# Kernel tuning notes

Hardware: AMD Instinct MI355X
Metric: run time of the kernel (lower is better)

Reference implementation:

```python
import jax, jax.numpy as jnp
import numpy as np

N_NODES = 100000
D = 256
E = 1000000
H = 128


def setup_inputs() -> dict:
    key = jax.random.key(0)
    k1, k2, k3, k4 = jax.random.split(key, 4)
    z = jax.random.normal(k1, (N_NODES, D), dtype=jnp.float32)
    edge_label_index = jax.random.randint(k2, (2, E), 0, N_NODES, dtype=jnp.int64)
    # Linear layers: PyTorch Linear(in, out) -> weight [out, in]; stored here as [in, out].
    W1 = jax.random.normal(k3, (2 * D, H), dtype=jnp.float32) * (1.0 / np.sqrt(2 * D))
    b1 = jnp.zeros((H,), dtype=jnp.float32)
    W2 = jax.random.normal(k4, (H, 1), dtype=jnp.float32) * (1.0 / np.sqrt(H))
    b2 = jnp.zeros((1,), dtype=jnp.float32)
    return {"z": z, "edge_label_index": edge_label_index,
            "W1": W1, "b1": b1, "W2": W2, "b2": b2}


def reference(z, edge_label_index, W1, b1, W2, b2):
    src = edge_label_index[0]
    dst = edge_label_index[1]
    # Gather node pairs and concat: [E, 2*D]
    pair = jnp.concatenate([z[src], z[dst]], axis=-1)
    h = jax.nn.relu(pair @ W1 + b1)          # [E, H]
    out = (h @ W2 + b2).reshape(-1)          # [E]
    return out
```

## Files before the change

### kernel.cpp

```cpp
#include <hip/hip_runtime.h>
#include <hip/hip_bf16.h>


typedef __attribute__((ext_vector_type(4))) float floatx4;
typedef __attribute__((ext_vector_type(8))) short short8;
typedef _Float16 half8v __attribute__((ext_vector_type(8)));

__device__ __forceinline__ unsigned short bf16rne(float x) {
    unsigned int u = __float_as_uint(x);
    u += 0x7fffu + ((u >> 16) & 1u);
    return (unsigned short)(u >> 16);
}

__device__ __forceinline__ void gl_lds16(const void* g, void* l) {
    __builtin_amdgcn_global_load_lds(
        (const __attribute__((address_space(1))) void*)(unsigned long long)g,
        (__attribute__((address_space(3))) void*)(unsigned)(unsigned long long)l,
        16, 0, 0);
}

__global__ void cvt_w1h(const float* __restrict__ W1, unsigned short* __restrict__ BTc2) {
    int t = blockIdx.x * blockDim.x + threadIdx.x;
    int hf = t >> 15, rem = t & 32767;
    int s = rem >> 12, rem2 = rem & 4095;
    int n = rem2 >> 5, rem3 = rem2 & 31;
    int gp = rem3 >> 3, j = rem3 & 7;
    int g = gp ^ ((n >> 1) & 3);
    int k = hf * 256 + s * 32 + g * 8 + j;
    BTc2[t] = bf16rne(W1[k * 128 + n]);
}

__global__ void cvt_w1(const float* __restrict__ W1, unsigned short* __restrict__ BTc) {
    int t = blockIdx.x * blockDim.x + threadIdx.x;
    int s = t >> 12, rem = t & 4095;
    int n = rem >> 5, rem2 = rem & 31;
    int gp = rem2 >> 3, j = rem2 & 7;
    int g = gp ^ ((n >> 1) & 3);
    int k = s * 32 + g * 8 + j;
    BTc[t] = bf16rne(W1[k * 128 + n]);
}

__global__ __launch_bounds__(256, 2)
void gemm_hb(const float* __restrict__ zf, int nnodes,
             const unsigned short* __restrict__ BTc2,
             const float* __restrict__ b1, _Float16* __restrict__ Hh)
{
    __shared__ unsigned short btile[2][2][2][128][32];

    const int t = threadIdx.x;
    const int wid = t >> 6;
    const int lane = t & 63;
    const int l15 = lane & 15;
    const int quad = lane >> 4;
    const int m0 = blockIdx.x * 128 + wid * 32;

    unsigned offs[2];
#pragma unroll
    for (int mf = 0; mf < 2; ++mf) {
        int r = m0 + mf * 16 + l15;
        r = r < nnodes ? r : nnodes - 1;
        offs[mf] = (unsigned)r * 1024u;
    }
    const char* zbb = (const char*)zf;

    const int swz = (l15 >> 1) & 3;
    const unsigned short* bbase = &btile[0][0][0][0][0] + l15 * 32 + (quad ^ swz) * 8;

    auto stage = [&](int kc, int buf) {
        char* lbase = (char*)&btile[0][0][0][0][0] + buf * 32768 + wid * 1024 + lane * 16;
        const char* gbase = (const char*)BTc2 + kc * 16384 + wid * 1024 + lane * 16;
#pragma unroll
        for (int h = 0; h < 2; ++h) {
            const char* g = gbase + h * 65536;
            char* l = lbase + h * 16384;
#pragma unroll
            for (int i = 0; i < 4; ++i)
                gl_lds16(g + i * 4096, l + i * 4096);
        }
    };

    auto load_a = [&](int ks, short8* dst) {
        const int cb = ks * 128 + quad * 32;
#pragma unroll
        for (int mf = 0; mf < 2; ++mf) {
            const float* pf = (const float*)(zbb + (size_t)offs[mf] + cb);
            float4 f0 = *(const float4*)pf;
            float4 f1 = *(const float4*)(pf + 4);
            short8 av;
            av[0] = (short)bf16rne(f0.x); av[1] = (short)bf16rne(f0.y);
            av[2] = (short)bf16rne(f0.z); av[3] = (short)bf16rne(f0.w);
            av[4] = (short)bf16rne(f1.x); av[5] = (short)bf16rne(f1.y);
            av[6] = (short)bf16rne(f1.z); av[7] = (short)bf16rne(f1.w);
            dst[mf] = av;
        }
    };

    floatx4 acc[2][16];
#pragma unroll
    for (int mf = 0; mf < 2; ++mf)
#pragma unroll
        for (int nf = 0; nf < 16; ++nf)
            acc[mf][nf] = (floatx4){0.f, 0.f, 0.f, 0.f};

    short8 A[3][2];
    stage(0, 0);
    load_a(0, A[0]);
    load_a(1, A[1]);
    __syncthreads();

#pragma unroll
    for (int kc = 0; kc < 4; ++kc) {
        if (kc < 3) stage(kc + 1, (kc + 1) & 1);

#pragma unroll
        for (int s4 = 0; s4 < 2; ++s4) {
            const int ks = kc * 2 + s4;
            if (ks + 2 < 8) load_a(ks + 2, A[(ks + 2) % 3]);

            const unsigned short* bs0 = bbase + (kc & 1) * 16384 + s4 * 4096;
            const short8* ac = A[ks % 3];

#pragma unroll
            for (int gq = 0; gq < 4; ++gq) {
                const unsigned short* bs = bs0 + (gq >> 1) * 8192 + (gq & 1) * 2048;
                short8 bfr[4];
#pragma unroll
                for (int nf = 0; nf < 4; ++nf)
                    bfr[nf] = *(const short8*)(bs + nf * 512);
#pragma unroll
                for (int nf = 0; nf < 4; ++nf)
#pragma unroll
                    for (int mf = 0; mf < 2; ++mf)
                        acc[mf][gq * 4 + nf] = __builtin_amdgcn_mfma_f32_16x16x32_bf16(
                            ac[mf], bfr[nf], acc[mf][gq * 4 + nf], 0, 0, 0);
            }
        }

        if (kc < 3) __syncthreads();
    }

    float b1v[8];
#pragma unroll
    for (int nf = 0; nf < 8; ++nf)
        b1v[nf] = b1[nf * 16 + l15];
#pragma unroll
    for (int mf = 0; mf < 2; ++mf) {
#pragma unroll
        for (int r = 0; r < 4; ++r) {
            int row = m0 + mf * 16 + quad * 4 + r;
            if (row < nnodes) {
                _Float16* hp = Hh + (size_t)row * 256 + l15;
#pragma unroll
                for (int nf = 0; nf < 8; ++nf)
                    hp[nf * 16] = (_Float16)(acc[mf][nf][r] + b1v[nf]);
#pragma unroll
                for (int nf = 0; nf < 8; ++nf)
                    hp[128 + nf * 16] = (_Float16)acc[mf][8 + nf][r];
            }
        }
    }
}

__global__ __launch_bounds__(256)
void edge_out(const _Float16* __restrict__ Hh, const int* __restrict__ eli,
              int E, int nnodes,
              const float* __restrict__ W2, const float* __restrict__ b2,
              float* __restrict__ out)
{
    const int t = threadIdx.x;
    const int lane = t & 63;
    const int wid = t >> 6;
    const int l15 = lane & 15;
    const int grp = lane >> 4;

    float w2v[8];
#pragma unroll
    for (int j = 0; j < 8; ++j)
        w2v[j] = W2[l15 * 8 + j];
    const float b2s = b2[0];

    const int e0 = blockIdx.x * 64 + wid * 16 + grp;

    half8v hs[4], hd[4];
    int ee[4];
#pragma unroll
    for (int i = 0; i < 4; ++i) {
        int e = e0 + i * 4;
        ee[i] = e;
        int ec = e < E ? e : E - 1;
        int s = eli[ec];
        int d = eli[E + ec];
        s = s < 0 ? 0 : (s >= nnodes ? nnodes - 1 : s);
        d = d < 0 ? 0 : (d >= nnodes ? nnodes - 1 : d);
        hs[i] = *(const half8v*)(Hh + (size_t)s * 256 + l15 * 8);
        hd[i] = *(const half8v*)(Hh + (size_t)d * 256 + 128 + l15 * 8);
    }
#pragma unroll
    for (int i = 0; i < 4; ++i) {
        float sacc = 0.f;
#pragma unroll
        for (int j = 0; j < 8; ++j) {
            float v = (float)hs[i][j] + (float)hd[i][j];
            v = v > 0.f ? v : 0.f;
            sacc = fmaf(v, w2v[j], sacc);
        }
        sacc += __shfl_xor(sacc, 1);
        sacc += __shfl_xor(sacc, 2);
        sacc += __shfl_xor(sacc, 4);
        sacc += __shfl_xor(sacc, 8);
        if (l15 == 0 && ee[i] < E)
            out[ee[i]] = sacc + b2s;
    }
}

__global__ __launch_bounds__(256, 2)
void fused_mlp_f32(const float* __restrict__ zf, const int* __restrict__ eli,
                   int E, int nnodes,
                   const unsigned short* __restrict__ BTc,
                   const float* __restrict__ b1, const float* __restrict__ W2,
                   const float* __restrict__ b2, float* __restrict__ out)
{
    __shared__ unsigned short btile[2][4][128][32];

    const int t = threadIdx.x;
    const int wid = t >> 6;
    const int lane = t & 63;
    const int l15 = lane & 15;
    const int quad = lane >> 4;
    const int m0 = blockIdx.x * 256 + wid * 64;

    unsigned offs[4], offd[4];
#pragma unroll
    for (int mf = 0; mf < 4; ++mf) {
        int e = m0 + mf * 16 + l15;
        e = e < E ? e : E - 1;
        int s = eli[e];
        int d = eli[E + e];
        s = s < 0 ? 0 : (s >= nnodes ? nnodes - 1 : s);
        d = d < 0 ? 0 : (d >= nnodes ? nnodes - 1 : d);
        offs[mf] = (unsigned)s * 1024u;
        offd[mf] = (unsigned)d * 1024u;
    }
    const char* zbb = (const char*)zf;

    const int swz = (l15 >> 1) & 3;
    const unsigned short* bbase = &btile[0][0][0][0] + l15 * 32 + (quad ^ swz) * 8;

    auto stage = [&](int kc, int buf) {
        const char* g = (const char*)BTc + kc * 32768 + wid * 1024 + lane * 16;
        char* l = (char*)&btile[buf][0][0][0] + wid * 1024 + lane * 16;
#pragma unroll
        for (int i = 0; i < 8; ++i)
            gl_lds16(g + i * 4096, l + i * 4096);
    };

    auto load_a = [&](int ks, short8* dst) {
        const unsigned* off = (ks < 8) ? offs : offd;
        const int cb = (ks & 7) * 128 + quad * 32;
#pragma unroll
        for (int mf = 0; mf < 4; ++mf) {
            const float* pf = (const float*)(zbb + (size_t)off[mf] + cb);
            float4 f0 = *(const float4*)pf;
            float4 f1 = *(const float4*)(pf + 4);
            short8 av;
            av[0] = (short)bf16rne(f0.x); av[1] = (short)bf16rne(f0.y);
            av[2] = (short)bf16rne(f0.z); av[3] = (short)bf16rne(f0.w);
            av[4] = (short)bf16rne(f1.x); av[5] = (short)bf16rne(f1.y);
            av[6] = (short)bf16rne(f1.z); av[7] = (short)bf16rne(f1.w);
            dst[mf] = av;
        }
    };

    floatx4 acc[4][8];
#pragma unroll
    for (int mf = 0; mf < 4; ++mf)
#pragma unroll
        for (int nf = 0; nf < 8; ++nf)
            acc[mf][nf] = (floatx4){0.f, 0.f, 0.f, 0.f};

    short8 A[3][4];
    stage(0, 0);
    load_a(0, A[0]);
    load_a(1, A[1]);
    __syncthreads();

#pragma unroll
    for (int kc = 0; kc < 4; ++kc) {
        if (kc < 3) stage(kc + 1, (kc + 1) & 1);

#pragma unroll
        for (int s4 = 0; s4 < 4; ++s4) {
            const int ks = kc * 4 + s4;
            if (ks + 2 < 16) load_a(ks + 2, A[(ks + 2) % 3]);

            const unsigned short* bs = bbase + (kc & 1) * 16384 + s4 * 4096;
            short8 bfr[8];
#pragma unroll
            for (int nf = 0; nf < 8; ++nf)
                bfr[nf] = *(const short8*)(bs + nf * 512);

            const short8* ac = A[ks % 3];
#pragma unroll
            for (int nf = 0; nf < 8; ++nf)
#pragma unroll
                for (int mf = 0; mf < 4; ++mf)
                    acc[mf][nf] = __builtin_amdgcn_mfma_f32_16x16x32_bf16(
                        ac[mf], bfr[nf], acc[mf][nf], 0, 0, 0);
        }

        if (kc < 3) __syncthreads();
    }

    const float b2s = b2[0];
    float b1v[8], w2v[8];
#pragma unroll
    for (int nf = 0; nf < 8; ++nf) {
        int c = nf * 16 + l15;
        b1v[nf] = b1[c];
        w2v[nf] = W2[c];
    }
#pragma unroll
    for (int mf = 0; mf < 4; ++mf) {
#pragma unroll
        for (int r = 0; r < 4; ++r) {
            float s = 0.f;
#pragma unroll
            for (int nf = 0; nf < 8; ++nf) {
                float v = acc[mf][nf][r] + b1v[nf];
                v = v > 0.f ? v : 0.f;
                s = fmaf(v, w2v[nf], s);
            }
            s += __shfl_xor(s, 1);
            s += __shfl_xor(s, 2);
            s += __shfl_xor(s, 4);
            s += __shfl_xor(s, 8);
            if (l15 == 0) {
                int e = m0 + mf * 16 + quad * 4 + r;
                if (e < E) out[e] = s + b2s;
            }
        }
    }
}

__global__ void naive_edge(const float* __restrict__ z, const int* __restrict__ eli,
                           int E, int nnodes,
                           const float* __restrict__ W1, const float* __restrict__ b1,
                           const float* __restrict__ W2, const float* __restrict__ b2,
                           float* __restrict__ out)
{
    __shared__ float red[2];
    int e = blockIdx.x;
    int j = threadIdx.x;
    int s = eli[e], d = eli[E + e];
    s = s < 0 ? 0 : (s >= nnodes ? nnodes - 1 : s);
    d = d < 0 ? 0 : (d >= nnodes ? nnodes - 1 : d);
    const float* zs = z + (long long)s * 256;
    const float* zd = z + (long long)d * 256;
    float h = b1[j];
    for (int i = 0; i < 256; ++i) h = fmaf(zs[i], W1[i * 128 + j], h);
    for (int i = 0; i < 256; ++i) h = fmaf(zd[i], W1[(256 + i) * 128 + j], h);
    h = h > 0.f ? h : 0.f;
    float v = h * W2[j];
    v += __shfl_xor(v, 1);  v += __shfl_xor(v, 2);  v += __shfl_xor(v, 4);
    v += __shfl_xor(v, 8);  v += __shfl_xor(v, 16); v += __shfl_xor(v, 32);
    if ((threadIdx.x & 63) == 0) red[threadIdx.x >> 6] = v;
    __syncthreads();
    if (threadIdx.x == 0) out[e] = red[0] + red[1] + b2[0];
}

extern "C" void kernel_launch(void* const* d_in, const int* in_sizes, int n_in,
                              void* d_out, int out_size, void* d_ws, size_t ws_size,
                              hipStream_t stream) {
    const float* z   = (const float*)d_in[0];
    const int*   eli = (const int*)d_in[1];
    const float* W1  = (const float*)d_in[2];
    const float* b1  = (const float*)d_in[3];
    const float* W2  = (const float*)d_in[4];
    const float* b2  = (const float*)d_in[5];
    float*       out = (float*)d_out;

    const int E      = in_sizes[1] / 2;
    const int nnodes = in_sizes[0] / 256;

    const size_t HB   = (size_t)nnodes * 512;
    const size_t BT2B = 131072;
    const size_t BTB  = (size_t)512 * 128 * 2;

    const int grid_gemm = (nnodes + 127) / 128;
    const int grid_edge = (E + 63) / 64;

    if (ws_size >= HB + BT2B) {
        _Float16*       Hh   = (_Float16*)d_ws;
        unsigned short* BTc2 = (unsigned short*)((char*)d_ws + HB);
        cvt_w1h<<<256, 256, 0, stream>>>(W1, BTc2);
        gemm_hb<<<grid_gemm, 256, 0, stream>>>(z, nnodes, BTc2, b1, Hh);
        edge_out<<<grid_edge, 256, 0, stream>>>(Hh, eli, E, nnodes, W2, b2, out);
    } else if (ws_size >= BTB) {
        unsigned short* BTc = (unsigned short*)d_ws;
        cvt_w1<<<256, 256, 0, stream>>>(W1, BTc);
        fused_mlp_f32<<<(E + 255) / 256, 256, 0, stream>>>(z, eli, E, nnodes, BTc, b1, W2, b2, out);
    } else {
        naive_edge<<<E, 128, 0, stream>>>(z, eli, E, nnodes, W1, b1, W2, b2, out);
    }
}
```

Baseline: 247.1 us.

## Read W1 fragments directly from global and use packed fp16 dot in edge kernel

The node GEMM stops staging the bf16 W1 tiles into LDS with async global-to-LDS copies and barriers. Each wave now loads its B fragments straight from global memory, relying on the small weight being L2/L1 resident, and deepens the A prefetch ring to four stages. The edge kernel does the add and relu in packed fp16 and accumulates with fdot2 against fp16-converted W2. This removes LDS traffic and syncs but adds redundant global loads per wave. It also lowers precision, since the add, relu and W2 now run in fp16.

```diff
diff --git a/kernel.cpp b/kernel.cpp
--- a/kernel.cpp
+++ b/kernel.cpp
@@ -5,6 +5,13 @@
 typedef __attribute__((ext_vector_type(4))) float floatx4;
 typedef __attribute__((ext_vector_type(8))) short short8;
 typedef _Float16 half8v __attribute__((ext_vector_type(8)));
+typedef __fp16 fp16x2 __attribute__((ext_vector_type(2)));
+
+#if defined(__has_builtin)
+#if __has_builtin(__builtin_amdgcn_fdot2)
+#define HAVE_FDOT2 1
+#endif
+#endif
 
 __device__ __forceinline__ unsigned short bf16rne(float x) {
     unsigned int u = __float_as_uint(x);
@@ -45,8 +52,6 @@
              const unsigned short* __restrict__ BTc2,
              const float* __restrict__ b1, _Float16* __restrict__ Hh)
 {
-    __shared__ unsigned short btile[2][2][2][128][32];
-
     const int t = threadIdx.x;
     const int wid = t >> 6;
     const int lane = t & 63;
@@ -64,20 +69,7 @@
     const char* zbb = (const char*)zf;
 
     const int swz = (l15 >> 1) & 3;
-    const unsigned short* bbase = &btile[0][0][0][0][0] + l15 * 32 + (quad ^ swz) * 8;
-
-    auto stage = [&](int kc, int buf) {
-        char* lbase = (char*)&btile[0][0][0][0][0] + buf * 32768 + wid * 1024 + lane * 16;
-        const char* gbase = (const char*)BTc2 + kc * 16384 + wid * 1024 + lane * 16;
-#pragma unroll
-        for (int h = 0; h < 2; ++h) {
-            const char* g = gbase + h * 65536;
-            char* l = lbase + h * 16384;
-#pragma unroll
-            for (int i = 0; i < 4; ++i)
-                gl_lds16(g + i * 4096, l + i * 4096);
-        }
-    };
+    const unsigned short* gb = BTc2 + l15 * 32 + (quad ^ swz) * 8;
 
     auto load_a = [&](int ks, short8* dst) {
         const int cb = ks * 128 + quad * 32;
@@ -102,41 +94,32 @@
         for (int nf = 0; nf < 16; ++nf)
             acc[mf][nf] = (floatx4){0.f, 0.f, 0.f, 0.f};
 
-    short8 A[3][2];
-    stage(0, 0);
+    short8 A[4][2];
     load_a(0, A[0]);
     load_a(1, A[1]);
-    __syncthreads();
-
-#pragma unroll
-    for (int kc = 0; kc < 4; ++kc) {
-        if (kc < 3) stage(kc + 1, (kc + 1) & 1);
-
-#pragma unroll
-        for (int s4 = 0; s4 < 2; ++s4) {
-            const int ks = kc * 2 + s4;
-            if (ks + 2 < 8) load_a(ks + 2, A[(ks + 2) % 3]);
-
-            const unsigned short* bs0 = bbase + (kc & 1) * 16384 + s4 * 4096;
-            const short8* ac = A[ks % 3];
-
-#pragma unroll
-            for (int gq = 0; gq < 4; ++gq) {
-                const unsigned short* bs = bs0 + (gq >> 1) * 8192 + (gq & 1) * 2048;
-                short8 bfr[4];
-#pragma unroll
-                for (int nf = 0; nf < 4; ++nf)
-                    bfr[nf] = *(const short8*)(bs + nf * 512);
-#pragma unroll
-                for (int nf = 0; nf < 4; ++nf)
-#pragma unroll
-                    for (int mf = 0; mf < 2; ++mf)
-                        acc[mf][gq * 4 + nf] = __builtin_amdgcn_mfma_f32_16x16x32_bf16(
-                            ac[mf], bfr[nf], acc[mf][gq * 4 + nf], 0, 0, 0);
-            }
-        }
-
-        if (kc < 3) __syncthreads();
+    load_a(2, A[2]);
+
+#pragma unroll
+    for (int ks = 0; ks < 8; ++ks) {
+        if (ks + 3 < 8) load_a(ks + 3, A[(ks + 3) & 3]);
+
+        const short8* ac = A[ks & 3];
+
+#pragma unroll
+        for (int gq = 0; gq < 4; ++gq) {
+            const unsigned short* bs =
+                gb + (gq >> 1) * 32768 + ks * 4096 + (gq & 1) * 2048;
+            short8 bfr[4];
+#pragma unroll
+            for (int nf = 0; nf < 4; ++nf)
+                bfr[nf] = *(const short8*)(bs + nf * 512);
+#pragma unroll
+            for (int nf = 0; nf < 4; ++nf)
+#pragma unroll
+                for (int mf = 0; mf < 2; ++mf)
+                    acc[mf][gq * 4 + nf] = __builtin_amdgcn_mfma_f32_16x16x32_bf16(
+                        ac[mf], bfr[nf], acc[mf][gq * 4 + nf], 0, 0, 0);
+        }
     }
 
     float b1v[8];
@@ -173,10 +156,12 @@
     const int l15 = lane & 15;
     const int grp = lane >> 4;
 
-    float w2v[8];
-#pragma unroll
-    for (int j = 0; j < 8; ++j)
-        w2v[j] = W2[l15 * 8 + j];
+    fp16x2 w2h[4];
+#pragma unroll
+    for (int p = 0; p < 4; ++p) {
+        w2h[p][0] = (__fp16)W2[l15 * 8 + 2 * p];
+        w2h[p][1] = (__fp16)W2[l15 * 8 + 2 * p + 1];
+    }
     const float b2s = b2[0];
 
     const int e0 = blockIdx.x * 64 + wid * 16 + grp;
@@ -195,15 +180,27 @@
         hs[i] = *(const half8v*)(Hh + (size_t)s * 256 + l15 * 8);
         hd[i] = *(const half8v*)(Hh + (size_t)d * 256 + 128 + l15 * 8);
     }
+    const half8v zero = {};
 #pragma unroll
     for (int i = 0; i < 4; ++i) {
+        half8v v = hs[i] + hd[i];
+        v = __builtin_elementwise_max(v, zero);
         float sacc = 0.f;
-#pragma unroll
-        for (int j = 0; j < 8; ++j) {
-            float v = (float)hs[i][j] + (float)hd[i][j];
-            v = v > 0.f ? v : 0.f;
-            sacc = fmaf(v, w2v[j], sacc);
-        }
+#if defined(HAVE_FDOT2)
+#pragma unroll
+        for (int p = 0; p < 4; ++p) {
+            fp16x2 a;
+            a[0] = (__fp16)v[2 * p];
+            a[1] = (__fp16)v[2 * p + 1];
+            sacc = __builtin_amdgcn_fdot2(a, w2h[p], sacc, false);
+        }
+#else
+#pragma unroll
+        for (int p = 0; p < 4; ++p) {
+            sacc = fmaf((float)v[2 * p],     (float)w2h[p][0], sacc);
+            sacc = fmaf((float)v[2 * p + 1], (float)w2h[p][1], sacc);
+        }
+#endif
         sacc += __shfl_xor(sacc, 1);
         sacc += __shfl_xor(sacc, 2);
         sacc += __shfl_xor(sacc, 4);
```

After: 284.4 us. 1.15x slower.
